# Optimization experiments

Measured on AMD Instinct MI355X. Metric: run time of the kernel, lower is better.

The kernel has to match this reference:

```python
import jax, jax.numpy as jnp
import numpy as np

B, C, H, W = 128, 3, 512, 512
P, NP, SCALE = 16, 3, 2          # patch_size, num_patches, scale
HG, HL = 256, 128                # hidden_g, hidden_l
D_IN = NP * C * P * P            # 2304


def _extract_patch(x, coords, size):
    # x: (B,C,H,W), coords: (B,2) int [x_coord, y_coord]; returns (B,C,size,size)
    pad = size // 2
    xp = jnp.pad(x, ((0, 0), (0, 0), (pad, pad), (pad, pad)))
    ch = xp.shape[1]

    def one(img, c):
        # slice [from_y:from_y+size, from_x:from_x+size]
        return jax.lax.dynamic_slice(img, (0, c[1], c[0]), (ch, size, size))

    return jax.vmap(one)(xp, coords)


def _foveate(x, l):
    h, w = x.shape[2], x.shape[3]
    # torch uses l.data (detached) and .long() truncation; values are >= 0
    coords = (0.5 * ((jax.lax.stop_gradient(l) + 1.0)
                     * jnp.array([h, w], jnp.float32))).astype(jnp.int32)
    patches = []
    size = P
    for _ in range(NP):
        p = _extract_patch(x, coords, size)
        if size > P:
            k = size // P  # avg_pool2d kernel = stride = k
            b, c = p.shape[0], p.shape[1]
            p = p.reshape(b, c, P, k, P, k).mean(axis=(3, 5))
        patches.append(p)
        size = int(SCALE * size)
    g = jnp.concatenate(patches, axis=1)  # (B, NP*C, P, P)
    return g.reshape(g.shape[0], -1)      # (B, D_IN)


def setup_inputs() -> dict:
    key = jax.random.key(0)
    ks = jax.random.split(key, 10)
    s = 0.02
    return {
        "x_t": jax.random.normal(ks[0], (B, C, H, W), jnp.float32),
        "l_t": jax.random.uniform(ks[1], (B, 2), jnp.float32, -1.0, 1.0),
        "w1": jax.random.normal(ks[2], (D_IN, HG), jnp.float32) * s,
        "b1": jnp.zeros((HG,), jnp.float32),
        "w2": jax.random.normal(ks[3], (2, HL), jnp.float32) * s,
        "b2": jnp.zeros((HL,), jnp.float32),
        "w3": jax.random.normal(ks[4], (HG, HG + HL), jnp.float32) * s,
        "b3": jnp.zeros((HG + HL,), jnp.float32),
        "w4": jax.random.normal(ks[5], (HL, HG + HL), jnp.float32) * s,
        "b4": jnp.zeros((HG + HL,), jnp.float32),
    }


def reference(x_t, l_t, w1, b1, w2, b2, w3, b3, w4, b4):
    glimpse = _foveate(x_t, l_t)                       # (B, D_IN)
    what = jax.nn.relu(glimpse @ w1 + b1) @ w3 + b3    # (B, HG+HL)
    where = jax.nn.relu(l_t @ w2 + b2) @ w4 + b4       # (B, HG+HL)
    return jax.nn.relu(what + where)
```

## Files before the change

### kernel.cpp

```cpp
#include <hip/hip_runtime.h>
#include <hip/hip_bf16.h>


#define B_    128
#define C_    3
#define H_    512
#define W_    512
#define P_    16
#define NP_   3
#define HG    256
#define HL    128
#define DIN   2304
#define HOUT  384

#define KS 36
#define BK 64
#define BM 32
#define BN 64

__global__ __launch_bounds__(256) void k1_foveate_where(
    const float* __restrict__ x, const float* __restrict__ l,
    const float* __restrict__ w2, const float* __restrict__ b2,
    const float* __restrict__ w4, const float* __restrict__ b4,
    float* __restrict__ glimpse, float* __restrict__ wherebuf)
{
    __shared__ float ld[64 * 64];
    const int bid = blockIdx.x;
    const int t   = threadIdx.x;

    if (bid < B_ * NP_ * C_) {
        const int b     = bid / (NP_ * C_);
        const int rem   = bid % (NP_ * C_);
        const int level = rem / C_;
        const int c     = rem % C_;

        const float l0 = l[b * 2 + 0];
        const float l1 = l[b * 2 + 1];
        int sx = (int)(((l0 + 1.0f) * 512.0f) * 0.5f);
        int sy = (int)(((l1 + 1.0f) * 512.0f) * 0.5f);
        sx = min(max(sx, 0), 512);
        sy = min(max(sy, 0), 512);

        const float* xc = x + (size_t)(b * C_ + c) * (H_ * W_);
        const int S   = P_ << level;
        const int pad = S >> 1;
        const int lg  = 4 + level;
        const int py  = t >> 4;
        const int px  = t & 15;

        float out;
        if (level == 0) {
            const int ry = sy - pad + py;
            const int rx = sx - pad + px;
            out = (ry >= 0 && ry < H_ && rx >= 0 && rx < W_) ? xc[ry * W_ + rx] : 0.0f;
        } else {
            const int n = S * S;
            for (int f = t; f < n; f += 256) {
                const int r  = f >> lg;
                const int cc = f & (S - 1);
                const int ry = sy - pad + r;
                const int rx = sx - pad + cc;
                ld[f] = (ry >= 0 && ry < H_ && rx >= 0 && rx < W_) ? xc[ry * W_ + rx] : 0.0f;
            }
            __syncthreads();
            float s = 0.0f;
            if (level == 1) {
                #pragma unroll
                for (int dy = 0; dy < 2; ++dy) {
                    const float2 v = *(const float2*)&ld[(py * 2 + dy) * 32 + px * 2];
                    s += v.x + v.y;
                }
                out = s * 0.25f;
            } else {
                #pragma unroll
                for (int dy = 0; dy < 4; ++dy) {
                    const float4 v = *(const float4*)&ld[(py * 4 + dy) * 64 + px * 4];
                    s += v.x + v.y + v.z + v.w;
                }
                out = s * 0.0625f;
            }
        }
        glimpse[(size_t)b * DIN + (level * C_ + c) * 256 + t] = out;
    } else {
        const int b = bid - B_ * NP_ * C_;
        const float l0 = l[b * 2 + 0];
        const float l1 = l[b * 2 + 1];
        if (t < HL) {
            const float v = l0 * w2[t] + l1 * w2[HL + t] + b2[t];
            ld[t] = fmaxf(v, 0.0f);
        }
        __syncthreads();
        for (int j = t; j < HOUT; j += 256) {
            float acc = b4[j];
            #pragma unroll 8
            for (int i = 0; i < HL; ++i) acc += ld[i] * w4[i * HOUT + j];
            wherebuf[b * HOUT + j] = acc;
        }
    }
}

__global__ __launch_bounds__(256) void k2_gemm1(
    const float* __restrict__ glimpse, const float* __restrict__ w1,
    float* __restrict__ partial)
{
    __shared__ float As[BM][BK + 4];
    __shared__ float Bs[BK][BN];

    const int bid = blockIdx.x;
    const int ks  = bid % KS;
    const int jb  = bid / KS;
    const int jt  = jb & 3;
    const int bt  = jb >> 2;
    const int t   = threadIdx.x;
    const int k0  = ks * BK;

    {
        int f = t;
        int row = f >> 4, c4 = f & 15;
        float4 v = *(const float4*)&glimpse[(size_t)(bt * BM + row) * DIN + k0 + c4 * 4];
        *(float4*)&As[row][c4 * 4] = v;
        f = t + 256;
        row = f >> 4; c4 = f & 15;
        float4 v2 = *(const float4*)&glimpse[(size_t)(bt * BM + row) * DIN + k0 + c4 * 4];
        *(float4*)&As[row][c4 * 4] = v2;
    }
    #pragma unroll
    for (int i = 0; i < 4; ++i) {
        const int f  = t + 256 * i;
        const int kr = f >> 4, c4 = f & 15;
        float4 v = *(const float4*)&w1[(size_t)(k0 + kr) * HG + jt * BN + c4 * 4];
        *(float4*)&Bs[kr][c4 * 4] = v;
    }
    __syncthreads();

    const int tx = t & 15;
    const int ty = t >> 4;
    float4 acc0 = {0.f, 0.f, 0.f, 0.f};
    float4 acc1 = {0.f, 0.f, 0.f, 0.f};
    #pragma unroll 8
    for (int k = 0; k < BK; ++k) {
        const float a0 = As[ty][k];
        const float a1 = As[ty + 16][k];
        const float4 bv = *(const float4*)&Bs[k][tx * 4];
        acc0.x += a0 * bv.x; acc0.y += a0 * bv.y; acc0.z += a0 * bv.z; acc0.w += a0 * bv.w;
        acc1.x += a1 * bv.x; acc1.y += a1 * bv.y; acc1.z += a1 * bv.z; acc1.w += a1 * bv.w;
    }
    float* p0 = &partial[((size_t)(ks * B_ + bt * BM + ty)) * HG + jt * BN + tx * 4];
    *(float4*)p0 = acc0;
    float* p1 = &partial[((size_t)(ks * B_ + bt * BM + ty + 16)) * HG + jt * BN + tx * 4];
    *(float4*)p1 = acc1;
}

__global__ __launch_bounds__(384) void k3_out(
    const float* __restrict__ partial, const float* __restrict__ b1,
    const float* __restrict__ w3, const float* __restrict__ b3,
    const float* __restrict__ wherebuf, float* __restrict__ out)
{
    __shared__ float hs[HG];
    const int b = blockIdx.x;
    const int t = threadIdx.x;

    if (t < HG) {
        float acc = b1[t];
        #pragma unroll 4
        for (int s = 0; s < KS; ++s)
            acc += partial[((size_t)(s * B_ + b)) * HG + t];
        hs[t] = fmaxf(acc, 0.0f);
    }
    __syncthreads();

    float acc = b3[t] + wherebuf[b * HOUT + t];
    #pragma unroll 8
    for (int i = 0; i < HG; ++i)
        acc += hs[i] * w3[i * HOUT + t];
    out[(size_t)b * HOUT + t] = fmaxf(acc, 0.0f);
}

extern "C" void kernel_launch(void* const* d_in, const int* in_sizes, int n_in,
                              void* d_out, int out_size, void* d_ws, size_t ws_size,
                              hipStream_t stream) {
    const float* x_t = (const float*)d_in[0];
    const float* l_t = (const float*)d_in[1];
    const float* w1  = (const float*)d_in[2];
    const float* b1  = (const float*)d_in[3];
    const float* w2  = (const float*)d_in[4];
    const float* b2  = (const float*)d_in[5];
    const float* w3  = (const float*)d_in[6];
    const float* b3  = (const float*)d_in[7];
    const float* w4  = (const float*)d_in[8];
    const float* b4  = (const float*)d_in[9];
    float* out = (float*)d_out;

    float* ws       = (float*)d_ws;
    float* glimpse  = ws;
    float* partial  = glimpse + (size_t)B_ * DIN;
    float* wherebuf = partial + (size_t)KS * B_ * HG;

    k1_foveate_where<<<B_ * NP_ * C_ + B_, 256, 0, stream>>>(
        x_t, l_t, w2, b2, w4, b4, glimpse, wherebuf);
    k2_gemm1<<<16 * KS, 256, 0, stream>>>(glimpse, w1, partial);
    k3_out<<<B_, 384, 0, stream>>>(partial, b1, w3, b3, wherebuf, out);
}
```

Measured before the change: 484.6 us.

## Share one 64x64 patch load across all pyramid levels and fuse where-path into output

The foveation kernel now loads a single 64x64 window per (batch, channel) into shared memory and derives all three pyramid levels from it, rather than fetching each level separately in its own block. The where-branch (l @ w2, relu, @ w4) moves out of the first kernel and into the output kernel, which removes the wherebuf round trip. The partial-sum reduction also uses four independent accumulators. The clamping of sx/sy was dropped, which is safe only because l lies in [-1,1].

```diff
diff --git a/kernel.cpp b/kernel.cpp
--- a/kernel.cpp
+++ b/kernel.cpp
@@ -7,7 +7,6 @@
 #define H_    512
 #define W_    512
 #define P_    16
-#define NP_   3
 #define HG    256
 #define HL    128
 #define DIN   2304
@@ -18,85 +17,55 @@
 #define BM 32
 #define BN 64
 
-__global__ __launch_bounds__(256) void k1_foveate_where(
+__global__ __launch_bounds__(256) void k1_foveate(
     const float* __restrict__ x, const float* __restrict__ l,
-    const float* __restrict__ w2, const float* __restrict__ b2,
-    const float* __restrict__ w4, const float* __restrict__ b4,
-    float* __restrict__ glimpse, float* __restrict__ wherebuf)
+    float* __restrict__ glimpse)
 {
     __shared__ float ld[64 * 64];
     const int bid = blockIdx.x;
-    const int t   = threadIdx.x;
+    const int b = bid / C_;
+    const int c = bid % C_;
+    const int t = threadIdx.x;
 
-    if (bid < B_ * NP_ * C_) {
-        const int b     = bid / (NP_ * C_);
-        const int rem   = bid % (NP_ * C_);
-        const int level = rem / C_;
-        const int c     = rem % C_;
+    const float l0 = l[b * 2 + 0];
+    const float l1 = l[b * 2 + 1];
+    const int sx = (int)(((l0 + 1.0f) * 512.0f) * 0.5f);
+    const int sy = (int)(((l1 + 1.0f) * 512.0f) * 0.5f);
 
-        const float l0 = l[b * 2 + 0];
-        const float l1 = l[b * 2 + 1];
-        int sx = (int)(((l0 + 1.0f) * 512.0f) * 0.5f);
-        int sy = (int)(((l1 + 1.0f) * 512.0f) * 0.5f);
-        sx = min(max(sx, 0), 512);
-        sy = min(max(sy, 0), 512);
+    const float* xc = x + (size_t)(b * C_ + c) * (H_ * W_);
 
-        const float* xc = x + (size_t)(b * C_ + c) * (H_ * W_);
-        const int S   = P_ << level;
-        const int pad = S >> 1;
-        const int lg  = 4 + level;
-        const int py  = t >> 4;
-        const int px  = t & 15;
+    for (int f = t; f < 64 * 64; f += 256) {
+        const int r  = f >> 6;
+        const int cc = f & 63;
+        const int ry = sy - 32 + r;
+        const int rx = sx - 32 + cc;
+        ld[f] = (ry >= 0 && ry < H_ && rx >= 0 && rx < W_) ? xc[ry * W_ + rx] : 0.0f;
+    }
+    __syncthreads();
 
-        float out;
-        if (level == 0) {
-            const int ry = sy - pad + py;
-            const int rx = sx - pad + px;
-            out = (ry >= 0 && ry < H_ && rx >= 0 && rx < W_) ? xc[ry * W_ + rx] : 0.0f;
-        } else {
-            const int n = S * S;
-            for (int f = t; f < n; f += 256) {
-                const int r  = f >> lg;
-                const int cc = f & (S - 1);
-                const int ry = sy - pad + r;
-                const int rx = sx - pad + cc;
-                ld[f] = (ry >= 0 && ry < H_ && rx >= 0 && rx < W_) ? xc[ry * W_ + rx] : 0.0f;
-            }
-            __syncthreads();
-            float s = 0.0f;
-            if (level == 1) {
-                #pragma unroll
-                for (int dy = 0; dy < 2; ++dy) {
-                    const float2 v = *(const float2*)&ld[(py * 2 + dy) * 32 + px * 2];
-                    s += v.x + v.y;
-                }
-                out = s * 0.25f;
-            } else {
-                #pragma unroll
-                for (int dy = 0; dy < 4; ++dy) {
-                    const float4 v = *(const float4*)&ld[(py * 4 + dy) * 64 + px * 4];
-                    s += v.x + v.y + v.z + v.w;
-                }
-                out = s * 0.0625f;
-            }
-        }
-        glimpse[(size_t)b * DIN + (level * C_ + c) * 256 + t] = out;
-    } else {
-        const int b = bid - B_ * NP_ * C_;
-        const float l0 = l[b * 2 + 0];
-        const float l1 = l[b * 2 + 1];
-        if (t < HL) {
-            const float v = l0 * w2[t] + l1 * w2[HL + t] + b2[t];
-            ld[t] = fmaxf(v, 0.0f);
-        }
-        __syncthreads();
-        for (int j = t; j < HOUT; j += 256) {
-            float acc = b4[j];
-            #pragma unroll 8
-            for (int i = 0; i < HL; ++i) acc += ld[i] * w4[i * HOUT + j];
-            wherebuf[b * HOUT + j] = acc;
-        }
+    const int py = t >> 4;
+    const int px = t & 15;
+
+    const float v0 = ld[(24 + py) * 64 + 24 + px];
+
+    float s1 = 0.0f;
+    #pragma unroll
+    for (int dy = 0; dy < 2; ++dy) {
+        const float2 v = *(const float2*)&ld[(16 + 2 * py + dy) * 64 + 16 + 2 * px];
+        s1 += v.x + v.y;
     }
+
+    float s2 = 0.0f;
+    #pragma unroll
+    for (int dy = 0; dy < 4; ++dy) {
+        const float4 v = *(const float4*)&ld[(py * 4 + dy) * 64 + px * 4];
+        s2 += v.x + v.y + v.z + v.w;
+    }
+
+    float* g = glimpse + (size_t)b * DIN;
+    g[(0 * C_ + c) * 256 + t] = v0;
+    g[(1 * C_ + c) * 256 + t] = s1 * 0.25f;
+    g[(2 * C_ + c) * 256 + t] = s2 * 0.0625f;
 }
 
 __global__ __launch_bounds__(256) void k2_gemm1(
@@ -154,25 +123,40 @@
 __global__ __launch_bounds__(384) void k3_out(
     const float* __restrict__ partial, const float* __restrict__ b1,
     const float* __restrict__ w3, const float* __restrict__ b3,
-    const float* __restrict__ wherebuf, float* __restrict__ out)
+    const float* __restrict__ l,  const float* __restrict__ w2,
+    const float* __restrict__ b2, const float* __restrict__ w4,
+    const float* __restrict__ b4, float* __restrict__ out)
 {
     __shared__ float hs[HG];
+    __shared__ float hl[HL];
     const int b = blockIdx.x;
     const int t = threadIdx.x;
 
     if (t < HG) {
-        float acc = b1[t];
-        #pragma unroll 4
-        for (int s = 0; s < KS; ++s)
-            acc += partial[((size_t)(s * B_ + b)) * HG + t];
-        hs[t] = fmaxf(acc, 0.0f);
+        float a0 = 0.f, a1 = 0.f, a2 = 0.f, a3 = 0.f;
+        #pragma unroll
+        for (int s = 0; s < KS; s += 4) {
+            a0 += partial[((size_t)((s + 0) * B_ + b)) * HG + t];
+            a1 += partial[((size_t)((s + 1) * B_ + b)) * HG + t];
+            a2 += partial[((size_t)((s + 2) * B_ + b)) * HG + t];
+            a3 += partial[((size_t)((s + 3) * B_ + b)) * HG + t];
+        }
+        hs[t] = fmaxf((a0 + a1) + (a2 + a3) + b1[t], 0.0f);
+    } else if (t < HG + HL) {
+        const int j = t - HG;
+        const float l0 = l[b * 2 + 0];
+        const float l1 = l[b * 2 + 1];
+        hl[j] = fmaxf(l0 * w2[j] + l1 * w2[HL + j] + b2[j], 0.0f);
     }
     __syncthreads();
 
-    float acc = b3[t] + wherebuf[b * HOUT + t];
+    float acc = b3[t] + b4[t];
     #pragma unroll 8
     for (int i = 0; i < HG; ++i)
         acc += hs[i] * w3[i * HOUT + t];
+    #pragma unroll 8
+    for (int i = 0; i < HL; ++i)
+        acc += hl[i] * w4[i * HOUT + t];
     out[(size_t)b * HOUT + t] = fmaxf(acc, 0.0f);
 }
 
@@ -191,13 +175,11 @@
     const float* b4  = (const float*)d_in[9];
     float* out = (float*)d_out;
 
-    float* ws       = (float*)d_ws;
-    float* glimpse  = ws;
-    float* partial  = glimpse + (size_t)B_ * DIN;
-    float* wherebuf = partial + (size_t)KS * B_ * HG;
+    float* ws      = (float*)d_ws;
+    float* glimpse = ws;
+    float* partial = glimpse + (size_t)B_ * DIN;
 
-    k1_foveate_where<<<B_ * NP_ * C_ + B_, 256, 0, stream>>>(
-        x_t, l_t, w2, b2, w4, b4, glimpse, wherebuf);
+    k1_foveate<<<B_ * C_, 256, 0, stream>>>(x_t, l_t, glimpse);
     k2_gemm1<<<16 * KS, 256, 0, stream>>>(glimpse, w1, partial);
-    k3_out<<<B_, 384, 0, stream>>>(partial, b1, w3, b3, wherebuf, out);
+    k3_out<<<B_, 384, 0, stream>>>(partial, b1, w3, b3, l_t, w2, b2, w4, b4, out);
 }
```

Measured after the change: 483.0 us. No clear change (-0.3%).
